# Kernel optimization log

Hardware: AMD Instinct MI355X
Metric: run time of the kernel (lower is better)

## Reference

```python
import jax, jax.numpy as jnp
import numpy as np

B, CIN, COUT, N, M, K = 8, 128, 256, 8192, 2048, 16
BN_EPS = 1e-5


def setup_inputs() -> dict:
    key = jax.random.key(0)
    k1, k2, k3 = jax.random.split(key, 3)
    x = jax.random.normal(k1, (B, CIN, N), dtype=jnp.float32)
    coords = jax.random.normal(k2, (B, 3, N), dtype=jnp.float32)
    W = jax.random.normal(k3, (COUT, CIN), dtype=jnp.float32) * 0.05  # 1x1 conv, bias=False
    gamma = jnp.ones((COUT,), dtype=jnp.float32)   # BatchNorm2d weight
    beta = jnp.zeros((COUT,), dtype=jnp.float32)   # BatchNorm2d bias
    return {"x": x, "coords": coords, "W": W, "gamma": gamma, "beta": beta}


def furthest_point_sampling(coords, num_samples):
    """coords: (B,3,N) -> indices (B,num_samples) int32. Greedy FPS starting at index 0."""
    pts = coords.transpose(0, 2, 1)  # (B,N,3)
    b, n, _ = pts.shape
    idx0 = jnp.zeros((b,), dtype=jnp.int32)
    mind0 = jnp.full((b, n), 1e10, dtype=pts.dtype)

    def step(carry, _):
        mind, last = carry
        lastpt = jnp.take_along_axis(pts, last[:, None, None], axis=1)  # (b,1,3)
        d = jnp.sum((pts - lastpt) ** 2, axis=-1)                        # (b,n)
        mind = jnp.minimum(mind, d)
        nxt = jnp.argmax(mind, axis=-1).astype(jnp.int32)
        return (mind, nxt), nxt

    (_, _), rest = jax.lax.scan(step, (mind0, idx0), None, length=num_samples - 1)
    return jnp.concatenate([idx0[:, None], rest.T], axis=1)  # (b,num_samples)


def reference(x, coords, W, gamma, beta):
    b = x.shape[0]
    fps_idx = furthest_point_sampling(coords, M)                # (B,M)
    pts = coords.transpose(0, 2, 1)                             # (B,N,3)
    bidx = jnp.arange(b)[:, None]
    fps_pts = pts[bidx, fps_idx]                                # (B,M,3)

    # squared-distance matrix via ||a||^2 + ||b||^2 - 2ab (avoids (B,M,N,3) temp)
    d = (jnp.sum(fps_pts ** 2, -1)[:, :, None]
         + jnp.sum(pts ** 2, -1)[:, None, :]
         - 2.0 * jnp.einsum('bmd,bnd->bmn', fps_pts, pts))      # (B,M,N)
    _, knn_idx = jax.lax.top_k(-d, K)                           # (B,M,K) nearest (sorted)

    x_t = x.transpose(0, 2, 1)                                  # (B,N,Cin)
    knn = x_t[jnp.arange(b)[:, None, None], knn_idx]            # (B,M,K,Cin)

    # PointwiseConv2D: 1x1 conv (no bias) + BatchNorm2d (batch stats) + ReLU
    h = jnp.einsum('bmkc,oc->bmko', knn, W)                     # (B,M,K,Cout)
    mean = jnp.mean(h, axis=(0, 1, 2))
    var = jnp.var(h, axis=(0, 1, 2))
    h = (h - mean) * jax.lax.rsqrt(var + BN_EPS) * gamma + beta
    h = jax.nn.relu(h)

    y = jnp.max(h, axis=2).transpose(0, 2, 1)                   # (B,Cout,M), max over k
    fps_coords = fps_pts.transpose(0, 2, 1)                     # (B,3,M)
    return y, fps_coords
```

## Files before the change

### kernel.cpp

```cpp
#include <hip/hip_runtime.h>
#include <math.h>

#define B_ 8
#define CIN_ 128
#define COUT_ 256
#define N_ 8192
#define M_ 2048
#define K_ 16

#define GEMM_BLOCKS 2048

__device__ __forceinline__ unsigned umax2(unsigned a, unsigned b) { return a > b ? a : b; }
__device__ __forceinline__ unsigned umin2(unsigned a, unsigned b) { return a < b ? a : b; }

__device__ __forceinline__ unsigned wave_reduce_umax(unsigned v) {
    v = umax2(v, (unsigned)__builtin_amdgcn_update_dpp(0, (int)v, 0x111, 0xf, 0xf, false));
    v = umax2(v, (unsigned)__builtin_amdgcn_update_dpp(0, (int)v, 0x112, 0xf, 0xf, false));
    v = umax2(v, (unsigned)__builtin_amdgcn_update_dpp(0, (int)v, 0x114, 0xf, 0xf, false));
    v = umax2(v, (unsigned)__builtin_amdgcn_update_dpp(0, (int)v, 0x118, 0xf, 0xf, false));
    v = umax2(v, (unsigned)__builtin_amdgcn_update_dpp(0, (int)v, 0x142, 0xf, 0xf, false));
    v = umax2(v, (unsigned)__builtin_amdgcn_update_dpp(0, (int)v, 0x143, 0xf, 0xf, false));
    return (unsigned)__builtin_amdgcn_readlane((int)v, 63);
}
__device__ __forceinline__ unsigned wave_reduce_umin(unsigned v) {
    v = umin2(v, (unsigned)__builtin_amdgcn_update_dpp(-1, (int)v, 0x111, 0xf, 0xf, false));
    v = umin2(v, (unsigned)__builtin_amdgcn_update_dpp(-1, (int)v, 0x112, 0xf, 0xf, false));
    v = umin2(v, (unsigned)__builtin_amdgcn_update_dpp(-1, (int)v, 0x114, 0xf, 0xf, false));
    v = umin2(v, (unsigned)__builtin_amdgcn_update_dpp(-1, (int)v, 0x118, 0xf, 0xf, false));
    v = umin2(v, (unsigned)__builtin_amdgcn_update_dpp(-1, (int)v, 0x142, 0xf, 0xf, false));
    v = umin2(v, (unsigned)__builtin_amdgcn_update_dpp(-1, (int)v, 0x143, 0xf, 0xf, false));
    return (unsigned)__builtin_amdgcn_readlane((int)v, 63);
}

__global__ __launch_bounds__(512) void fps_gemm_kernel(const float* __restrict__ coords,
                                                       const float* __restrict__ x,
                                                       const float* __restrict__ W,
                                                       float* __restrict__ fpts,
                                                       float* __restrict__ out_fps,
                                                       float* __restrict__ hp) {
    __shared__ union {
        struct {
            float4 pts[N_];
            unsigned long long kbuf[2][8];
            int wlist[M_];
        } f;
        struct {
            float Xs[64][128];
            float Wt[64][68];
        } g;
    } sm;

    const int tid = threadIdx.x;

    if (blockIdx.x < B_) {
#pragma clang fp contract(off)
        const int b = blockIdx.x;
        const int lane = tid & 63;
        const int wid = tid >> 6;
        const float* cb = coords + (size_t)b * 3 * N_;
        float4* pts = sm.f.pts;
        unsigned long long (*kbuf)[8] = sm.f.kbuf;
        int* wlist = sm.f.wlist;

        float px[16], py[16], pz[16], mind[16];
#pragma unroll
        for (int s = 0; s < 16; ++s) {
            int p = tid + s * 512;
            px[s] = cb[p];
            py[s] = cb[N_ + p];
            pz[s] = cb[2 * N_ + p];
            mind[s] = 1e10f;
            pts[p] = make_float4(px[s], py[s], pz[s], 0.f);
        }
        __syncthreads();
        float4 p0 = pts[0];
        float lx = p0.x, ly = p0.y, lz = p0.z;

        int par = 0;
        for (int m = 1; m < M_; ++m) {
            float bv = -1.0f; int bs = 0;
#pragma unroll
            for (int s = 0; s < 16; ++s) {
                float dx = px[s] - lx;
                float dy = py[s] - ly;
                float dz = pz[s] - lz;
                float d = __builtin_fmaf(dz, dz, __builtin_fmaf(dy, dy, dx * dx));
                float mn = fminf(mind[s], d);
                mind[s] = mn;
                if (mn > bv) { bv = mn; bs = s; }
            }
            int bi = tid + bs * 512;
            unsigned kd = __float_as_uint(bv);
            unsigned md = wave_reduce_umax(kd);
            unsigned cand = (kd == md) ? (unsigned)bi : 0xffffffffu;
            unsigned mi = wave_reduce_umin(cand);
            if (lane == 0)
                kbuf[par][wid] = ((unsigned long long)md << 32) |
                                 (unsigned long long)(0xffffffffu - mi);
            __syncthreads();
            const unsigned long long* kb = kbuf[par];
            ulonglong2 q0 = *(const ulonglong2*)&kb[0];
            ulonglong2 q1 = *(const ulonglong2*)&kb[2];
            ulonglong2 q2 = *(const ulonglong2*)&kb[4];
            ulonglong2 q3 = *(const ulonglong2*)&kb[6];
            unsigned long long a0 = q0.x > q0.y ? q0.x : q0.y;
            unsigned long long a1 = q1.x > q1.y ? q1.x : q1.y;
            unsigned long long a2 = q2.x > q2.y ? q2.x : q2.y;
            unsigned long long a3 = q3.x > q3.y ? q3.x : q3.y;
            unsigned long long b01 = a0 > a1 ? a0 : a1;
            unsigned long long b23 = a2 > a3 ? a2 : a3;
            unsigned long long best = b01 > b23 ? b01 : b23;
            int widx = (int)(0xffffffffu - (unsigned)(best & 0xffffffffull));
            widx = ((unsigned)widx < (unsigned)N_) ? widx : 0;
            float4 wp = pts[widx];
            lx = wp.x; ly = wp.y; lz = wp.z;
            if (tid == 0) wlist[m] = widx;
            par ^= 1;
        }

        __syncthreads();
        for (int mm = tid; mm < M_; mm += 512) {
            int wi = (mm == 0) ? 0 : wlist[mm];
            wi = ((unsigned)wi < (unsigned)N_) ? wi : 0;
            float4 wp = pts[wi];
            ((float4*)fpts)[b * M_ + mm] = make_float4(wp.x, wp.y, wp.z, 0.f);
            out_fps[(size_t)b * 3 * M_ + 0 * M_ + mm] = wp.x;
            out_fps[(size_t)b * 3 * M_ + 1 * M_ + mm] = wp.y;
            out_fps[(size_t)b * 3 * M_ + 2 * M_ + mm] = wp.z;
        }
    } else {
        const int gb = blockIdx.x - B_;
        const int b = gb >> 8;
        const int rem = gb & 255;
        const int n0 = (rem >> 2) * 128;
        const int o0 = (rem & 3) * 64;
        const int tn = (tid & 31) * 4;
        const int to = (tid >> 5) * 4;
        const float* xg = x + (size_t)b * CIN_ * N_;
        float (*Xs)[128] = sm.g.Xs;
        float (*Wt)[68] = sm.g.Wt;

        float acc[4][4] = {};
        for (int kk = 0; kk < CIN_; kk += 64) {
#pragma unroll
            for (int i = 0; i < 16; ++i) {
                int e = tid + 512 * i;
                int r = e >> 7, q = e & 127;
                Xs[r][q] = xg[(size_t)(kk + r) * N_ + n0 + q];
            }
#pragma unroll
            for (int i = 0; i < 8; ++i) {
                int e = tid + 512 * i;
                int r = e >> 6, q = e & 63;
                Wt[q][r] = W[(size_t)(o0 + r) * CIN_ + kk + q];
            }
            __syncthreads();
#pragma unroll 8
            for (int c = 0; c < 64; ++c) {
                float4 a = *(const float4*)&Xs[c][tn];
                float4 bb = *(const float4*)&Wt[c][to];
                float av[4] = {a.x, a.y, a.z, a.w};
                float bv[4] = {bb.x, bb.y, bb.z, bb.w};
#pragma unroll
                for (int j = 0; j < 4; ++j)
#pragma unroll
                    for (int l = 0; l < 4; ++l)
                        acc[j][l] += av[j] * bv[l];
            }
            __syncthreads();
        }
#pragma unroll
        for (int j = 0; j < 4; ++j) {
            float4 v = make_float4(acc[j][0], acc[j][1], acc[j][2], acc[j][3]);
            *(float4*)&hp[((size_t)b * N_ + n0 + tn + j) * COUT_ + o0 + to] = v;
        }
    }
}

__global__ __launch_bounds__(256) void knn_kernel(const float* __restrict__ coords,
                                                  const float* __restrict__ fpts,
                                                  int* __restrict__ knn) {
#pragma clang fp contract(off)
    const int bidx = blockIdx.x;
    const int b = bidx >> 9;
    const int mg = bidx & 511;
    const int tid = threadIdx.x;
    const int lane = tid & 63;
    const int w = tid >> 6;
    const int m = mg * 4 + w;
    const int row = b * M_ + m;
    const float* cb = coords + (size_t)b * 3 * N_;

    __shared__ float4 tile[1024];

    float4 f = ((const float4*)fpts)[row];
    const float fx = f.x, fy = f.y, fz = f.z;
    const float sf = __builtin_fmaf(fz, fz, __builtin_fmaf(fy, fy, fx * fx));

    float ed = INFINITY; int ei = 0x7fffffff;
    float tau_d = INFINITY; int tau_i = 0x7fffffff;

    for (int t = 0; t < 8; ++t) {
        const int base = t * 1024;
#pragma unroll
        for (int j = 0; j < 4; ++j) {
            int idx = tid + 256 * j;
            int n = base + idx;
            float gx = cb[n], gy = cb[N_ + n], gz = cb[2 * N_ + n];
            float sp = __builtin_fmaf(gz, gz, __builtin_fmaf(gy, gy, gx * gx));
            tile[idx] = make_float4(gx, gy, gz, sp);
        }
        __syncthreads();
        for (int s = 0; s < 16; ++s) {
            int l = s * 64 + lane;
            float4 p = tile[l];
            int n = base + l;
            float dot = __builtin_fmaf(fz, p.z, __builtin_fmaf(fy, p.y, fx * p.x));
            float d = (sf + p.w) - 2.0f * dot;
            bool q = (d < tau_d) || (d == tau_d && n < tau_i);
            unsigned long long bal = __ballot(q);
            while (bal) {
                int lb = __ffsll(bal) - 1;
                bal &= bal - 1;
                float dv = __shfl(d, lb);
                int   iv = __shfl(n, lb);
                if ((dv < tau_d) || (dv == tau_d && iv < tau_i)) {
                    float pud = __shfl_up(ed, 1);
                    int   pui = __shfl_up(ei, 1);
                    bool cs = (dv < ed) || (dv == ed && iv < ei);
                    bool cp = (lane != 0) && ((dv < pud) || (dv == pud && iv < pui));
                    ed = cs ? (cp ? pud : dv) : ed;
                    ei = cs ? (cp ? pui : iv) : ei;
                    tau_d = __shfl(ed, 15);
                    tau_i = __shfl(ei, 15);
                }
            }
        }
        __syncthreads();
    }
    if (lane < K_) {
        int v = ei;
        knn[(size_t)row * K_ + lane] = ((unsigned)v < (unsigned)N_) ? v : 0;
    }
}

__global__ __launch_bounds__(256) void stats_partial_kernel(const float* __restrict__ hp,
                                                            const int* __restrict__ knn,
                                                            double* __restrict__ partial,
                                                            double* __restrict__ partial2) {
    const int o = threadIdx.x;
    const int g0 = blockIdx.x * 1024;
    double s = 0.0, s2 = 0.0;
    for (int r = 0; r < 1024; ++r) {
        int g = g0 + r;
        int row = g >> 4;
        int k = g & 15;
        int b = row >> 11;
        int n = knn[row * K_ + k];
        n = ((unsigned)n < (unsigned)N_) ? n : 0;
        double h = (double)hp[((size_t)b * N_ + n) * COUT_ + o];
        s += h;
        s2 += h * h;
    }
    partial[(size_t)blockIdx.x * 256 + o] = s;
    partial2[(size_t)blockIdx.x * 256 + o] = s2;
}

__global__ void bn_final_kernel(const double* __restrict__ partial,
                                const double* __restrict__ partial2,
                                const float* __restrict__ gamma,
                                const float* __restrict__ beta,
                                float* __restrict__ scale,
                                float* __restrict__ bias) {
    int o = threadIdx.x;
    double s = 0.0, s2 = 0.0;
    for (int j = 0; j < 256; ++j) {
        s += partial[(size_t)j * 256 + o];
        s2 += partial2[(size_t)j * 256 + o];
    }
    const double inv = 1.0 / (double)(B_ * M_ * K_);
    double mean = s * inv;
    double var = s2 * inv - mean * mean;
    if (var < 0.0) var = 0.0;
    double r = 1.0 / sqrt(var + 1e-5);
    double g = (double)gamma[o];
    scale[o] = (float)(r * g);
    bias[o] = (float)((double)beta[o] - mean * r * g);
}

__global__ __launch_bounds__(256) void finalize_kernel(const float* __restrict__ hp,
                                                       const int* __restrict__ knn,
                                                       const float* __restrict__ scale,
                                                       const float* __restrict__ bias,
                                                       float* __restrict__ y) {
    const int b = blockIdx.x >> 6;
    const int m0 = (blockIdx.x & 63) * 32;
    const int tid = threadIdx.x;
    __shared__ int kidx[512];
    __shared__ float tile[32][257];

    for (int e = tid; e < 512; e += 256) {
        int n = knn[(b * M_ + m0 + (e >> 4)) * K_ + (e & 15)];
        kidx[e] = ((unsigned)n < (unsigned)N_) ? n : 0;
    }
    __syncthreads();

    const float s = scale[tid];
    const float t = bias[tid];
    const float* hb = hp + (size_t)b * N_ * COUT_;
    for (int mm = 0; mm < 32; ++mm) {
        float v = -INFINITY;
#pragma unroll
        for (int k = 0; k < K_; ++k) {
            int n = kidx[mm * 16 + k];
            float h = hb[(size_t)n * COUT_ + tid];
            v = fmaxf(v, h * s + t);
        }
        v = fmaxf(v, 0.0f);
        tile[mm][tid] = v;
    }
    __syncthreads();
#pragma unroll
    for (int r = 0; r < 32; ++r) {
        int o2 = r * 8 + (tid >> 5);
        int mm = tid & 31;
        y[((size_t)b * COUT_ + o2) * M_ + m0 + mm] = tile[mm][o2];
    }
}

__global__ void sentinel_kernel(float* out, float v) { out[0] = v; }

extern "C" void kernel_launch(void* const* d_in, const int* in_sizes, int n_in,
                              void* d_out, int out_size, void* d_ws, size_t ws_size,
                              hipStream_t stream) {
    const float* x = (const float*)d_in[0];
    const float* coords = (const float*)d_in[1];
    const float* W = (const float*)d_in[2];
    const float* gamma = (const float*)d_in[3];
    const float* beta = (const float*)d_in[4];
    float* y = (float*)d_out;
    float* out_fps = y + (size_t)B_ * COUT_ * M_;

    if (n_in != 5 ||
        in_sizes[0] != B_ * CIN_ * N_ ||
        in_sizes[1] != B_ * 3 * N_ ||
        in_sizes[2] != COUT_ * CIN_ ||
        in_sizes[3] != COUT_ || in_sizes[4] != COUT_ ||
        out_size != B_ * COUT_ * M_ + B_ * 3 * M_) {
        sentinel_kernel<<<1, 1, 0, stream>>>(y, -2.0e6f);
        return;
    }

    const size_t HP_BYTES = (size_t)B_ * N_ * COUT_ * 4;
    const size_t FPTS_BYTES = (size_t)B_ * M_ * 16;
    const size_t KNN_BYTES = (size_t)B_ * M_ * K_ * 4;
    const size_t PART_BYTES = (size_t)256 * 256 * 8;
    const size_t NEED = HP_BYTES + FPTS_BYTES + KNN_BYTES + 2 * PART_BYTES + 8192;
    if (ws_size < NEED) {
        sentinel_kernel<<<1, 1, 0, stream>>>(y, -1.0e6f);
        return;
    }
    char* ws = (char*)d_ws;
    float* hp = (float*)ws;
    float* fpts = (float*)(ws + HP_BYTES);
    int* knn = (int*)(ws + HP_BYTES + FPTS_BYTES);
    double* partial = (double*)(ws + HP_BYTES + FPTS_BYTES + KNN_BYTES);
    double* partial2 = (double*)(ws + HP_BYTES + FPTS_BYTES + KNN_BYTES + PART_BYTES);
    float* scale = (float*)(ws + HP_BYTES + FPTS_BYTES + KNN_BYTES + 2 * PART_BYTES);
    float* bias = scale + 256;

    fps_gemm_kernel<<<B_ + GEMM_BLOCKS, 512, 0, stream>>>(coords, x, W, fpts, out_fps, hp);
    knn_kernel<<<B_ * 512, 256, 0, stream>>>(coords, fpts, knn);
    stats_partial_kernel<<<256, 256, 0, stream>>>(hp, knn, partial, partial2);
    bn_final_kernel<<<1, 256, 0, stream>>>(partial, partial2, gamma, beta, scale, bias);
    finalize_kernel<<<512, 256, 0, stream>>>(hp, knn, scale, bias, y);
}
```

Measured before the change: 1.896 ms.

## Compute BN statistics from per-point neighbor multiplicity histogram instead of gathers

The kNN kernel now atomically counts how often each source point is selected as a neighbor. The BN stats kernel then walks hp rows once per point, weighting the sum and sum of squares by that count, instead of gathering 262144 random rows. The GEMM blocks zero the counts array. This swaps the random gather traffic for a coalesced sequential pass plus atomics. It adds a workspace buffer and relies on the zeroing finishing before the kNN kernel runs, which stream order guarantees.

```diff
diff --git a/kernel.cpp b/kernel.cpp
--- a/kernel.cpp
+++ b/kernel.cpp
@@ -37,7 +37,8 @@
                                                        const float* __restrict__ W,
                                                        float* __restrict__ fpts,
                                                        float* __restrict__ out_fps,
-                                                       float* __restrict__ hp) {
+                                                       float* __restrict__ hp,
+                                                       int* __restrict__ counts) {
     __shared__ union {
         struct {
             float4 pts[N_];
@@ -130,6 +131,8 @@
         }
     } else {
         const int gb = blockIdx.x - B_;
+        if (tid < 32) counts[gb * 32 + tid] = 0;
+
         const int b = gb >> 8;
         const int rem = gb & 255;
         const int n0 = (rem >> 2) * 128;
@@ -179,7 +182,8 @@
 
 __global__ __launch_bounds__(256) void knn_kernel(const float* __restrict__ coords,
                                                   const float* __restrict__ fpts,
-                                                  int* __restrict__ knn) {
+                                                  int* __restrict__ knn,
+                                                  int* __restrict__ counts) {
 #pragma clang fp contract(off)
     const int bidx = blockIdx.x;
     const int b = bidx >> 9;
@@ -240,27 +244,29 @@
     }
     if (lane < K_) {
         int v = ei;
-        knn[(size_t)row * K_ + lane] = ((unsigned)v < (unsigned)N_) ? v : 0;
+        v = ((unsigned)v < (unsigned)N_) ? v : 0;
+        knn[(size_t)row * K_ + lane] = v;
+        atomicAdd(&counts[b * N_ + v], 1);
     }
 }
 
 __global__ __launch_bounds__(256) void stats_partial_kernel(const float* __restrict__ hp,
-                                                            const int* __restrict__ knn,
+                                                            const int* __restrict__ counts,
                                                             double* __restrict__ partial,
                                                             double* __restrict__ partial2) {
     const int o = threadIdx.x;
-    const int g0 = blockIdx.x * 1024;
+    const int base = blockIdx.x * 256;
     double s = 0.0, s2 = 0.0;
-    for (int r = 0; r < 1024; ++r) {
-        int g = g0 + r;
-        int row = g >> 4;
-        int k = g & 15;
-        int b = row >> 11;
-        int n = knn[row * K_ + k];
-        n = ((unsigned)n < (unsigned)N_) ? n : 0;
-        double h = (double)hp[((size_t)b * N_ + n) * COUT_ + o];
-        s += h;
-        s2 += h * h;
+    for (int r = 0; r < 256; ++r) {
+        int g = base + r;
+        int cnt = counts[g];
+        if (cnt) {
+            double h = (double)hp[(size_t)g * COUT_ + o];
+            double c = (double)cnt;
+            double ch = c * h;
+            s += ch;
+            s2 += ch * h;
+        }
     }
     partial[(size_t)blockIdx.x * 256 + o] = s;
     partial2[(size_t)blockIdx.x * 256 + o] = s2;
@@ -355,7 +361,8 @@
     const size_t FPTS_BYTES = (size_t)B_ * M_ * 16;
     const size_t KNN_BYTES = (size_t)B_ * M_ * K_ * 4;
     const size_t PART_BYTES = (size_t)256 * 256 * 8;
-    const size_t NEED = HP_BYTES + FPTS_BYTES + KNN_BYTES + 2 * PART_BYTES + 8192;
+    const size_t CNT_BYTES = (size_t)B_ * N_ * 4;
+    const size_t NEED = HP_BYTES + FPTS_BYTES + KNN_BYTES + 2 * PART_BYTES + CNT_BYTES + 8192;
     if (ws_size < NEED) {
         sentinel_kernel<<<1, 1, 0, stream>>>(y, -1.0e6f);
         return;
@@ -366,12 +373,13 @@
     int* knn = (int*)(ws + HP_BYTES + FPTS_BYTES);
     double* partial = (double*)(ws + HP_BYTES + FPTS_BYTES + KNN_BYTES);
     double* partial2 = (double*)(ws + HP_BYTES + FPTS_BYTES + KNN_BYTES + PART_BYTES);
-    float* scale = (float*)(ws + HP_BYTES + FPTS_BYTES + KNN_BYTES + 2 * PART_BYTES);
+    int* counts = (int*)(ws + HP_BYTES + FPTS_BYTES + KNN_BYTES + 2 * PART_BYTES);
+    float* scale = (float*)(ws + HP_BYTES + FPTS_BYTES + KNN_BYTES + 2 * PART_BYTES + CNT_BYTES);
     float* bias = scale + 256;
 
-    fps_gemm_kernel<<<B_ + GEMM_BLOCKS, 512, 0, stream>>>(coords, x, W, fpts, out_fps, hp);
-    knn_kernel<<<B_ * 512, 256, 0, stream>>>(coords, fpts, knn);
-    stats_partial_kernel<<<256, 256, 0, stream>>>(hp, knn, partial, partial2);
+    fps_gemm_kernel<<<B_ + GEMM_BLOCKS, 512, 0, stream>>>(coords, x, W, fpts, out_fps, hp, counts);
+    knn_kernel<<<B_ * 512, 256, 0, stream>>>(coords, fpts, knn, counts);
+    stats_partial_kernel<<<256, 256, 0, stream>>>(hp, counts, partial, partial2);
     bn_final_kernel<<<1, 256, 0, stream>>>(partial, partial2, gamma, beta, scale, bias);
     finalize_kernel<<<512, 256, 0, stream>>>(hp, knn, scale, bias, y);
 }
```

New measurement: 1.900 ms. About the same (+0.2%).
